# Kernel optimization log

Hardware: AMD Instinct MI355X
Metric: run time of the kernel (lower is better)

Reference implementation:

```python
import jax, jax.numpy as jnp
import numpy as np

HIDDEN = 4096
NH = 32          # num attention heads
NKV = 8          # num key/value heads
HD = HIDDEN // NH  # 128
THETA = 10000.0
WINDOW = 4096    # sliding window hard-coded in forward


def _rotate_half(x):
    x1, x2 = jnp.split(x, 2, axis=-1)
    return jnp.concatenate((-x2, x1), axis=-1)


def setup_inputs() -> dict:
    key = jax.random.key(0)
    ks = jax.random.split(key, 5)
    B, S = 1, 2048
    hidden_states = jax.random.normal(ks[0], (B, S, HIDDEN), jnp.float32)
    position_ids = jnp.broadcast_to(jnp.arange(S, dtype=jnp.int64), (B, S))
    s = 0.02
    q_w = jax.random.normal(ks[1], (HIDDEN, NH * HD), jnp.float32) * s
    k_w = jax.random.normal(ks[2], (HIDDEN, NKV * HD), jnp.float32) * s
    v_w = jax.random.normal(ks[3], (HIDDEN, NKV * HD), jnp.float32) * s
    o_w = jax.random.normal(ks[4], (NH * HD, HIDDEN), jnp.float32) * s
    return {"hidden_states": hidden_states, "position_ids": position_ids,
            "q_w": q_w, "k_w": k_w, "v_w": v_w, "o_w": o_w}


def reference(hidden_states, position_ids, q_w, k_w, v_w, o_w):
    B, S, _ = hidden_states.shape
    # projections (bias=False), split heads -> [B, H, S, D]
    q = (hidden_states @ q_w).reshape(B, S, NH, HD).transpose(0, 2, 1, 3)
    k = (hidden_states @ k_w).reshape(B, S, NKV, HD).transpose(0, 2, 1, 3)
    v = (hidden_states @ v_w).reshape(B, S, NKV, HD).transpose(0, 2, 1, 3)

    # rotary embedding cache (MistralRotaryEmbedding)
    inv_freq = 1.0 / (THETA ** (jnp.arange(0, HD, 2, dtype=jnp.float32) / HD))
    t = jnp.arange(S, dtype=jnp.float32)
    freqs = t[:, None] * inv_freq[None, :]           # [S, HD/2]
    emb = jnp.concatenate((freqs, freqs), axis=-1)   # [S, HD]
    cos = jnp.cos(emb)[position_ids][:, None]        # [B, 1, S, HD]
    sin = jnp.sin(emb)[position_ids][:, None]
    q = q * cos + _rotate_half(q) * sin
    k = k * cos + _rotate_half(k) * sin

    # GQA repeat_kv: [B, NKV, S, D] -> [B, NH, S, D]
    rep = NH // NKV
    k = jnp.repeat(k, rep, axis=1)
    v = jnp.repeat(v, rep, axis=1)

    # scores + sliding-window causal mask
    scale = 1.0 / np.sqrt(HD).astype(np.float32)
    w = jnp.einsum("bhqd,bhkd->bhqk", q, k) * scale  # [B, NH, S, S]
    i = jnp.arange(S)[:, None]
    j = jnp.arange(S)[None, :]
    allowed = (j <= i) & ((i - j) < WINDOW)
    neg = jnp.finfo(jnp.float32).min
    w = w + jnp.where(allowed, 0.0, neg)[None, None]

    # fp32 softmax (upcast as in HF Mistral)
    w = jax.nn.softmax(w.astype(jnp.float32), axis=-1).astype(q.dtype)

    out = jnp.einsum("bhqk,bhkd->bhqd", w, v)        # [B, NH, S, D]
    out = out.transpose(0, 2, 1, 3).reshape(B, S, NH * HD)
    return out @ o_w                                  # [B, S, HIDDEN]
```

## Files before the change

### kernel.cpp

```cpp
#include <hip/hip_runtime.h>
#include <hip/hip_bf16.h>

#define S 2048
#define HID 4096
#define NH 32
#define NKV 8
#define HD 128
#define QKVN 6144

typedef __attribute__((ext_vector_type(8))) short bf16x8;
typedef __attribute__((ext_vector_type(4))) float f32x4;
typedef __attribute__((ext_vector_type(8))) unsigned short u16x8;
typedef __attribute__((ext_vector_type(4))) unsigned short u16x4;

#define GLOAD16(src, dst)                                                        \
  __builtin_amdgcn_global_load_lds(                                              \
      (const __attribute__((address_space(1))) unsigned int*)(src),              \
      (__attribute__((address_space(3))) unsigned int*)(dst), 16, 0, 0)

__device__ __forceinline__ unsigned short f2bf(float f) {
  union { float f; unsigned u; } c; c.f = f;
  unsigned u = c.u;
  return (unsigned short)((u + 0x7FFFu + ((u >> 16) & 1u)) >> 16);
}
__device__ __forceinline__ float bf2f(unsigned short h) {
  union { unsigned u; float f; } c; c.u = ((unsigned)h) << 16;
  return c.f;
}

__global__ void convert_kernel(const float* __restrict__ in,
                               unsigned short* __restrict__ out, int n4) {
  int i = blockIdx.x * blockDim.x + threadIdx.x;
  if (i < n4) {
    float4 v = ((const float4*)in)[i];
    ushort4 o;
    o.x = f2bf(v.x); o.y = f2bf(v.y); o.z = f2bf(v.z); o.w = f2bf(v.w);
    ((ushort4*)out)[i] = o;
  }
}

__global__ void transpose_convert(const float* __restrict__ in,
                                  unsigned short* __restrict__ out, int N) {
  __shared__ float tile[32][33];
  int tx = threadIdx.x, ty = threadIdx.y;
  int n0 = blockIdx.x * 32, k0 = blockIdx.y * 32;
#pragma unroll
  for (int i = 0; i < 32; i += 8)
    tile[ty + i][tx] = in[(size_t)(k0 + ty + i) * N + n0 + tx];
  __syncthreads();
#pragma unroll
  for (int i = 0; i < 32; i += 8)
    out[(size_t)(n0 + ty + i) * HID + k0 + tx] = f2bf(tile[tx][ty + i]);
}

__device__ __forceinline__ void storeC(unsigned short* C, size_t idx, float v) { C[idx] = f2bf(v); }
__device__ __forceinline__ void storeC(float* C, size_t idx, float v) { C[idx] = v; }

template <typename OutT>
__launch_bounds__(256, 4)
__global__ void gemm_bt(const unsigned short* __restrict__ A,
                        const unsigned short* __restrict__ Bt,
                        OutT* __restrict__ C, int K, int ldc) {
  __shared__ unsigned short As[2][128 * 32];
  __shared__ unsigned short Bs[2][128 * 32];
  const int tid = threadIdx.x, lane = tid & 63, w = tid >> 6;
  const int wr = w >> 1, wc = w & 1;

  const int gx = gridDim.x;
  const int lin = blockIdx.y * gx + blockIdx.x;
  const int cpx = (gx * gridDim.y) >> 3;
  const int swz = (lin & 7) * cpx + (lin >> 3);
  const int m0 = (swz / gx) * 128, n0 = (swz % gx) * 128;

  const int lq = lane & 15, g = lane >> 4;

  f32x4 acc[4][4] = {};

  auto STAGE = [&](int b, int kt) {
#pragma unroll
    for (int i = 0; i < 2; ++i) {
      int row = w * 32 + i * 16 + (lane >> 2);
      int ch = (lane & 3) * 8;
      GLOAD16(A + (size_t)(m0 + row) * K + kt + ch, &As[b][(w * 2 + i) * 512]);
      GLOAD16(Bt + (size_t)(n0 + row) * K + kt + ch, &Bs[b][(w * 2 + i) * 512]);
    }
  };

  STAGE(0, 0);
  __syncthreads();
  int cur = 0;
  for (int kt = 0; kt < K; kt += 32) {
    if (kt + 32 < K) STAGE(cur ^ 1, kt + 32);
    bf16x8 af[4], bfr[4];
#pragma unroll
    for (int mi = 0; mi < 4; ++mi)
      af[mi] = *(const bf16x8*)&As[cur][(wr * 64 + mi * 16 + lq) * 32 + g * 8];
#pragma unroll
    for (int ni = 0; ni < 4; ++ni)
      bfr[ni] = *(const bf16x8*)&Bs[cur][(wc * 64 + ni * 16 + lq) * 32 + g * 8];
#pragma unroll
    for (int mi = 0; mi < 4; ++mi)
#pragma unroll
      for (int ni = 0; ni < 4; ++ni)
        acc[mi][ni] = __builtin_amdgcn_mfma_f32_16x16x32_bf16(af[mi], bfr[ni], acc[mi][ni], 0, 0, 0);
    __syncthreads();
    cur ^= 1;
  }

#pragma unroll
  for (int mi = 0; mi < 4; ++mi) {
#pragma unroll
    for (int ni = 0; ni < 4; ++ni) {
      int row = m0 + wr * 64 + mi * 16 + g * 4;
      int col = n0 + wc * 64 + ni * 16 + lq;
#pragma unroll
      for (int r = 0; r < 4; ++r)
        storeC(C, (size_t)(row + r) * ldc + col, acc[mi][ni][r]);
    }
  }
}

template <typename OutT>
__launch_bounds__(512, 1)
__global__ void gemm256_bt(const unsigned short* __restrict__ A,
                           const unsigned short* __restrict__ Bt,
                           OutT* __restrict__ C, int K, int ldc) {
  __shared__ unsigned short As[2][2][256 * 32];
  __shared__ unsigned short Bs[2][2][256 * 32];
  const int tid = threadIdx.x, lane = tid & 63, w = tid >> 6;
  const int wm = w >> 2, wn = w & 3;
  const int m0 = blockIdx.y * 256, n0 = blockIdx.x * 256;
  const int lq = lane & 15, g = lane >> 4;
  const int swz8 = (g ^ (lq & 3)) << 3;

  f32x4 acc[8][4] = {};
  const int NT = K >> 6;

  auto STAGE_PAIR = [&](int bb, int ss, int kt) {
#pragma unroll
    for (int i = 0; i < 2; ++i) {
      int ci = tid + i * 512;
      int row = ci >> 2;
      int jl = ((ci & 3) ^ (row & 3)) << 3;
      GLOAD16(A + (size_t)(m0 + row) * K + kt + ss * 32 + jl, &As[bb][ss][ci * 8]);
      GLOAD16(Bt + (size_t)(n0 + row) * K + kt + ss * 32 + jl, &Bs[bb][ss][ci * 8]);
    }
  };

  STAGE_PAIR(0, 0, 0);
  STAGE_PAIR(0, 1, 0);

  for (int t = 0; t < NT; ++t) {
    const int c = t & 1;
    const bool more = (t + 1) < NT;
    const int kt1 = (t + 1) << 6;
#pragma unroll
    for (int s = 0; s < 2; ++s) {
      if (s == 0 || more) asm volatile("s_waitcnt vmcnt(4)" ::: "memory");
      else                asm volatile("s_waitcnt vmcnt(0)" ::: "memory");
      __builtin_amdgcn_s_barrier();

      bf16x8 af[8], bf[4];
#pragma unroll
      for (int mi = 0; mi < 8; ++mi)
        af[mi] = *(const bf16x8*)&As[c][s][(wm * 128 + mi * 16 + lq) * 32 + swz8];
#pragma unroll
      for (int ni = 0; ni < 4; ++ni)
        bf[ni] = *(const bf16x8*)&Bs[c][s][(wn * 64 + ni * 16 + lq) * 32 + swz8];

      if (more) STAGE_PAIR(c ^ 1, s, kt1);

      asm volatile("s_waitcnt lgkmcnt(0)" ::: "memory");
      __builtin_amdgcn_sched_barrier(0);
      __builtin_amdgcn_s_setprio(1);
#pragma unroll
      for (int mi = 0; mi < 8; ++mi)
#pragma unroll
        for (int ni = 0; ni < 4; ++ni)
          acc[mi][ni] = __builtin_amdgcn_mfma_f32_16x16x32_bf16(af[mi], bf[ni], acc[mi][ni], 0, 0, 0);
      __builtin_amdgcn_s_setprio(0);
    }
  }

#pragma unroll
  for (int mi = 0; mi < 8; ++mi)
#pragma unroll
    for (int ni = 0; ni < 4; ++ni) {
      int row = m0 + wm * 128 + mi * 16 + g * 4;
      int col = n0 + wn * 64 + ni * 16 + lq;
#pragma unroll
      for (int r = 0; r < 4; ++r)
        storeC(C, (size_t)(row + r) * ldc + col, acc[mi][ni][r]);
    }
}

__global__ void rope_kernel(unsigned short* __restrict__ qkv) {
  int idx = blockIdx.x * blockDim.x + threadIdx.x;
  int d = idx & 63;
  int h = (idx >> 6) % (NH + NKV);
  int s = (idx >> 6) / (NH + NKV);
  size_t base = (size_t)s * QKVN + (h < NH ? h * HD : NH * HD + (h - NH) * HD);
  float invf = __expf(-(float)d * (1.0f / 64.0f) * 9.210340371976184f);
  float ang = (float)s * invf;
  float c, sn;
  __sincosf(ang, &sn, &c);
  float x1 = bf2f(qkv[base + d]);
  float x2 = bf2f(qkv[base + d + 64]);
  float o1 = x1 * c - x2 * sn;
  float o2 = x2 * c + x1 * sn;
  if (h < NH) {
    o1 *= 0.08838834764831845f;
    o2 *= 0.08838834764831845f;
  }
  qkv[base + d] = f2bf(o1);
  qkv[base + d + 64] = f2bf(o2);
}

__launch_bounds__(512, 4)
__global__ void attn_kernel(const unsigned short* __restrict__ qkv,
                            unsigned short* __restrict__ ao) {
  __shared__ unsigned short Ks[2][64 * 128];
  __shared__ unsigned short Vt[128 * 88];
  __shared__ unsigned short Ps[8][16 * 88];

  const int tid = threadIdx.x, lane = tid & 63, w = tid >> 6;
  const int b = blockIdx.x;
  const int h = blockIdx.y;
  const int qblk = (h < 16) ? (15 - b) : b;
  const int kh = h >> 2;
  const int lq = lane & 15, g = lane >> 4;
  const int qbase = qblk * 128 + w * 16;
  const size_t koff = (size_t)NH * HD + (size_t)kh * HD;
  const size_t voff = (size_t)(NH + NKV) * HD + (size_t)kh * HD;

  bf16x8 qf[4];
  {
    const unsigned short* qp = qkv + (size_t)(qbase + lq) * QKVN + (size_t)h * HD + g * 8;
#pragma unroll
    for (int ks = 0; ks < 4; ++ks) qf[ks] = *(const bf16x8*)(qp + ks * 32);
  }

  f32x4 o[8] = {};
  float m = -1e30f;
  float l = 0.f;

  auto KSTAGE = [&](int bb, int kv0) {
#pragma unroll
    for (int i = 0; i < 2; ++i) {
      int kvk = (w * 2 + i) * 4 + (lane >> 4);
      int chl = (lane & 15) ^ (kvk & 7);
      GLOAD16(qkv + (size_t)(kv0 + kvk) * QKVN + koff + chl * 8, &Ks[bb][(w * 2 + i) * 512]);
    }
  };
  const int vd0 = (tid & 31) * 4;
  const int vkv = (tid >> 5) * 4;
  u16x4 vr[4];
  auto VLOAD = [&](int kv0) {
#pragma unroll
    for (int i = 0; i < 4; ++i)
      vr[i] = *(const u16x4*)(qkv + (size_t)(kv0 + vkv + i) * QKVN + voff + vd0);
  };
  auto VWRITE = [&]() {
#pragma unroll
    for (int j = 0; j < 4; ++j) {
      const int d = vd0 + j;
      const int vswz = ((d >> 3) & 3) << 1;
      const int vcol = (((vkv >> 2) ^ vswz) << 2);
      u16x4 val = {vr[0][j], vr[1][j], vr[2][j], vr[3][j]};
      *(u16x4*)&Vt[d * 88 + vcol] = val;
    }
  };

  unsigned short* Pw = &Ps[w][0];
  const int nt = qblk * 2 + 2;

  KSTAGE(0, 0);
  VLOAD(0);
  int cur = 0;
  for (int t = 0; t < nt; ++t) {
    const int kv0 = t * 64;
    __syncthreads();
    VWRITE();
    __syncthreads();
    if (t + 1 < nt) { KSTAGE(cur ^ 1, kv0 + 64); VLOAD(kv0 + 64); }

    const int nraw = qbase + 16 - kv0;
    const int nact = nraw > 64 ? 64 : nraw;

    f32x4 sc[4];
    __builtin_amdgcn_s_setprio(1);
#pragma unroll
    for (int st = 0; st < 4; ++st) {
      if (st * 16 < nact) {
        f32x4 s = {};
#pragma unroll
        for (int ks = 0; ks < 4; ++ks) {
          const bf16x8 kf = *(const bf16x8*)
              &Ks[cur][(st * 16 + lq) * 128 + (((ks * 4 + g) ^ (lq & 7)) << 3)];
          s = __builtin_amdgcn_mfma_f32_16x16x32_bf16(kf, qf[ks], s, 0, 0, 0);
        }
        sc[st] = s;
      } else {
        sc[st] = (f32x4){-1e30f, -1e30f, -1e30f, -1e30f};
      }
    }
    __builtin_amdgcn_s_setprio(0);
    if (nraw < 79) {
      const int q = qbase + lq;
#pragma unroll
      for (int st = 0; st < 4; ++st) {
        int kv = kv0 + st * 16 + g * 4;
#pragma unroll
        for (int r = 0; r < 4; ++r)
          if (kv + r > q) sc[st][r] = -1e30f;
      }
    }

    float mn = fmaxf(fmaxf(fmaxf(sc[0][0], sc[0][1]), fmaxf(sc[0][2], sc[0][3])),
                     fmaxf(fmaxf(sc[1][0], sc[1][1]), fmaxf(sc[1][2], sc[1][3])));
    mn = fmaxf(mn, fmaxf(fmaxf(fmaxf(sc[2][0], sc[2][1]), fmaxf(sc[2][2], sc[2][3])),
                         fmaxf(fmaxf(sc[3][0], sc[3][1]), fmaxf(sc[3][2], sc[3][3]))));
    mn = fmaxf(mn, __shfl_xor(mn, 16, 64));
    mn = fmaxf(mn, __shfl_xor(mn, 32, 64));
    const bool need = __any(mn > m);
    const float m2 = fmaxf(m, mn);
    const float alpha = __expf(m - m2);
    m = m2;
    float rs = 0.f;
#pragma unroll
    for (int st = 0; st < 4; ++st)
#pragma unroll
      for (int r = 0; r < 4; ++r) {
        float p = __expf(sc[st][r] - m2);
        sc[st][r] = p;
        rs += p;
      }
    rs += __shfl_xor(rs, 16, 64);
    rs += __shfl_xor(rs, 32, 64);
    l = l * alpha + rs;

    if (need) {
      float alphaR[4];
#pragma unroll
      for (int r = 0; r < 4; ++r) alphaR[r] = __shfl(alpha, g * 4 + r, 64);
#pragma unroll
      for (int p = 0; p < 8; ++p)
#pragma unroll
        for (int r = 0; r < 4; ++r) o[p][r] *= alphaR[r];
    }

#pragma unroll
    for (int st = 0; st < 4; ++st) {
      u16x4 val = {f2bf(sc[st][0]), f2bf(sc[st][1]), f2bf(sc[st][2]), f2bf(sc[st][3])};
      *(u16x4*)&Pw[lq * 88 + st * 16 + g * 4] = val;
    }

    const int nks = nact > 0 ? (nact + 31) >> 5 : 0;
    __builtin_amdgcn_s_setprio(1);
    for (int ks = 0; ks < nks; ++ks) {
      const bf16x8 pf = *(const bf16x8*)&Pw[lq * 88 + ks * 32 + g * 8];
#pragma unroll
      for (int p = 0; p < 8; ++p) {
        const int d = p * 16 + lq;
        const int rswz = ((d >> 3) & 3) << 1;
        const int kvc = (ks * 8 + g * 2) ^ rswz;
        const bf16x8 vf = *(const bf16x8*)&Vt[d * 88 + (kvc << 2)];
        o[p] = __builtin_amdgcn_mfma_f32_16x16x32_bf16(pf, vf, o[p], 0, 0, 0);
      }
    }
    __builtin_amdgcn_s_setprio(0);

    cur ^= 1;
  }

  float invR[4];
#pragma unroll
  for (int r = 0; r < 4; ++r) invR[r] = 1.0f / __shfl(l, g * 4 + r, 64);
#pragma unroll
  for (int p = 0; p < 8; ++p)
#pragma unroll
    for (int r = 0; r < 4; ++r)
      ao[(size_t)(qbase + g * 4 + r) * (NH * HD) + (size_t)h * HD + p * 16 + lq] =
          f2bf(o[p][r] * invR[r]);
}

extern "C" void kernel_launch(void* const* d_in, const int* in_sizes, int n_in,
                              void* d_out, int out_size, void* d_ws, size_t ws_size,
                              hipStream_t stream) {
  const float* X  = (const float*)d_in[0];
  const float* qw = (const float*)d_in[2];
  const float* kw = (const float*)d_in[3];
  const float* vw = (const float*)d_in[4];
  const float* ow = (const float*)d_in[5];
  float* out = (float*)d_out;

  char* ws = (char*)d_ws;
  unsigned short* Xb  = (unsigned short*)(ws);
  unsigned short* Wt  = (unsigned short*)(ws + (size_t)(16u << 20));
  unsigned short* QKV = (unsigned short*)(ws + (size_t)(64u << 20));
  unsigned short* AO  = (unsigned short*)(ws + (size_t)(88u << 20));
  unsigned short* OWt = (unsigned short*)(ws);

  dim3 tb(32, 8);

  convert_kernel<<<(S * HID / 4 + 255) / 256, 256, 0, stream>>>(X, Xb, S * HID / 4);
  transpose_convert<<<dim3(HID / 32, HID / 32), tb, 0, stream>>>(qw, Wt, HID);
  transpose_convert<<<dim3((NKV * HD) / 32, HID / 32), tb, 0, stream>>>(kw, Wt + (size_t)(NH * HD) * HID, NKV * HD);
  transpose_convert<<<dim3((NKV * HD) / 32, HID / 32), tb, 0, stream>>>(vw, Wt + (size_t)(NH + NKV) * HD * HID, NKV * HD);
  gemm256_bt<unsigned short><<<dim3(QKVN / 256, S / 256), 512, 0, stream>>>(Xb, Wt, QKV, HID, QKVN);
  transpose_convert<<<dim3(HID / 32, HID / 32), tb, 0, stream>>>(ow, OWt, HID);
  rope_kernel<<<(S * (NH + NKV) * 64) / 256, 256, 0, stream>>>(QKV);
  attn_kernel<<<dim3(16, NH), 512, 0, stream>>>(QKV, AO);
  gemm_bt<float><<<dim3(HID / 128, S / 128), 256, 0, stream>>>(AO, OWt, out, HID, HID);
}
```

Measured before the change: 354.6 us.

## Restructure gemm_bt pipeline with swizzled LDS, 64-wide K stages and manual waitcnt

Reworks the 128x128 bf16 GEMM main loop to stage two 32-wide K sub-tiles per iteration into double-buffered LDS. Fine-grained vmcnt waits and raw barriers replace __syncthreads, and MFMA sections get raised wave priority. LDS chunks are XOR-swizzled to cut bank conflicts on fragment reads. The block-index grouping swizzle for L2 locality is dropped. LDS use doubles and launch bounds fall to 2 blocks per SM, trading occupancy for deeper prefetch.

```diff
diff --git a/kernel.cpp b/kernel.cpp
--- a/kernel.cpp
+++ b/kernel.cpp
@@ -57,54 +57,65 @@
 __device__ __forceinline__ void storeC(float* C, size_t idx, float v) { C[idx] = v; }
 
 template <typename OutT>
-__launch_bounds__(256, 4)
+__launch_bounds__(256, 2)
 __global__ void gemm_bt(const unsigned short* __restrict__ A,
                         const unsigned short* __restrict__ Bt,
                         OutT* __restrict__ C, int K, int ldc) {
-  __shared__ unsigned short As[2][128 * 32];
-  __shared__ unsigned short Bs[2][128 * 32];
+  __shared__ unsigned short As[2][2][128 * 32];
+  __shared__ unsigned short Bs[2][2][128 * 32];
   const int tid = threadIdx.x, lane = tid & 63, w = tid >> 6;
   const int wr = w >> 1, wc = w & 1;
-
-  const int gx = gridDim.x;
-  const int lin = blockIdx.y * gx + blockIdx.x;
-  const int cpx = (gx * gridDim.y) >> 3;
-  const int swz = (lin & 7) * cpx + (lin >> 3);
-  const int m0 = (swz / gx) * 128, n0 = (swz % gx) * 128;
-
+  const int m0 = blockIdx.y * 128, n0 = blockIdx.x * 128;
   const int lq = lane & 15, g = lane >> 4;
+  const int swz8 = (g ^ (lq & 3) ^ ((lq >> 2) & 3)) << 3;
 
   f32x4 acc[4][4] = {};
-
-  auto STAGE = [&](int b, int kt) {
+  const int NT = K >> 6;
+
+  auto STAGE_PAIR = [&](int bb, int ss, int kt) {
 #pragma unroll
     for (int i = 0; i < 2; ++i) {
-      int row = w * 32 + i * 16 + (lane >> 2);
-      int ch = (lane & 3) * 8;
-      GLOAD16(A + (size_t)(m0 + row) * K + kt + ch, &As[b][(w * 2 + i) * 512]);
-      GLOAD16(Bt + (size_t)(n0 + row) * K + kt + ch, &Bs[b][(w * 2 + i) * 512]);
+      int ci = tid + i * 256;
+      int row = ci >> 2;
+      int jl = (((ci & 3) ^ (row & 3) ^ ((row >> 2) & 3))) << 3;
+      GLOAD16(A + (size_t)(m0 + row) * K + kt + ss * 32 + jl, &As[bb][ss][ci * 8]);
+      GLOAD16(Bt + (size_t)(n0 + row) * K + kt + ss * 32 + jl, &Bs[bb][ss][ci * 8]);
     }
   };
 
-  STAGE(0, 0);
-  __syncthreads();
-  int cur = 0;
-  for (int kt = 0; kt < K; kt += 32) {
-    if (kt + 32 < K) STAGE(cur ^ 1, kt + 32);
-    bf16x8 af[4], bfr[4];
-#pragma unroll
-    for (int mi = 0; mi < 4; ++mi)
-      af[mi] = *(const bf16x8*)&As[cur][(wr * 64 + mi * 16 + lq) * 32 + g * 8];
-#pragma unroll
-    for (int ni = 0; ni < 4; ++ni)
-      bfr[ni] = *(const bf16x8*)&Bs[cur][(wc * 64 + ni * 16 + lq) * 32 + g * 8];
-#pragma unroll
-    for (int mi = 0; mi < 4; ++mi)
+  STAGE_PAIR(0, 0, 0);
+  STAGE_PAIR(0, 1, 0);
+
+  for (int t = 0; t < NT; ++t) {
+    const int c = t & 1;
+    const bool more = (t + 1) < NT;
+    const int kt1 = (t + 1) << 6;
+#pragma unroll
+    for (int s = 0; s < 2; ++s) {
+      if (s == 0 || more) asm volatile("s_waitcnt vmcnt(4)" ::: "memory");
+      else                asm volatile("s_waitcnt vmcnt(0)" ::: "memory");
+      __builtin_amdgcn_s_barrier();
+
+      bf16x8 af[4], bfr[4];
+#pragma unroll
+      for (int mi = 0; mi < 4; ++mi)
+        af[mi] = *(const bf16x8*)&As[c][s][(wr * 64 + mi * 16 + lq) * 32 + swz8];
 #pragma unroll
       for (int ni = 0; ni < 4; ++ni)
-        acc[mi][ni] = __builtin_amdgcn_mfma_f32_16x16x32_bf16(af[mi], bfr[ni], acc[mi][ni], 0, 0, 0);
-    __syncthreads();
-    cur ^= 1;
+        bfr[ni] = *(const bf16x8*)&Bs[c][s][(wc * 64 + ni * 16 + lq) * 32 + swz8];
+
+      if (more) STAGE_PAIR(c ^ 1, s, kt1);
+
+      asm volatile("s_waitcnt lgkmcnt(0)" ::: "memory");
+      __builtin_amdgcn_sched_barrier(0);
+      __builtin_amdgcn_s_setprio(1);
+#pragma unroll
+      for (int mi = 0; mi < 4; ++mi)
+#pragma unroll
+        for (int ni = 0; ni < 4; ++ni)
+          acc[mi][ni] = __builtin_amdgcn_mfma_f32_16x16x32_bf16(af[mi], bfr[ni], acc[mi][ni], 0, 0, 0);
+      __builtin_amdgcn_s_setprio(0);
+    }
   }
 
 #pragma unroll
```

Measured after the change: 331.5 us. 6.5% less time.
